# Performance work log

Hardware: AMD Instinct MI355X
Metric: run time of the kernel (lower is better)

## Reference

```python
import jax, jax.numpy as jnp
import numpy as np

NUM_HEADS = 8
EPS = 1e-12  # torch F.normalize default eps


def _l2_normalize(t, axis):
    n = jnp.sqrt(jnp.sum(t * t, axis=axis, keepdims=True))
    return t / jnp.maximum(n, EPS)


def setup_inputs() -> dict:
    key = jax.random.key(0)
    k1, k2, k3 = jax.random.split(key, 3)
    B, N, D = 32, 3136, 384
    x = jax.random.normal(k1, (B, N, D), dtype=jnp.float32)
    qkv_w = jax.random.normal(k2, (3 * D, D), dtype=jnp.float32) * (1.0 / np.sqrt(D))
    temperature = jnp.ones((NUM_HEADS, 1, 1), dtype=jnp.float32)
    proj_w = jax.random.normal(k3, (D, D), dtype=jnp.float32) * (1.0 / np.sqrt(D))
    proj_b = jnp.zeros((D,), dtype=jnp.float32)
    return {"x": x, "qkv_w": qkv_w, "temperature": temperature,
            "proj_w": proj_w, "proj_b": proj_b}


def reference(x, qkv_w, temperature, proj_w, proj_b):
    B, N, D = x.shape
    H = NUM_HEADS
    C = D // H
    # qkv projection (no bias), split last dim as (3, H, C) -> (3, B, H, C, N)
    qkv = jnp.einsum('bnd,ed->bne', x, qkv_w)
    qkv = qkv.reshape(B, N, 3, H, C).transpose(2, 0, 3, 4, 1)
    q, k, v = qkv[0], qkv[1], qkv[2]            # each (B, H, C, N)
    q = _l2_normalize(q, axis=-1)               # normalize over tokens N
    k = _l2_normalize(k, axis=-1)
    # cross-covariance attention: (B, H, C, C), scaled by per-head temperature
    attn = jnp.einsum('bhcn,bhdn->bhcd', q, k) * temperature
    attn = jax.nn.softmax(attn, axis=-1)
    out = jnp.einsum('bhcd,bhdn->bhcn', attn, v)  # (B, H, C, N)
    out = out.transpose(0, 3, 1, 2).reshape(B, N, D)
    return jnp.einsum('bnd,ed->bne', out, proj_w) + proj_b
```

## Files before the change

### kernel.cpp

```cpp
#include <hip/hip_runtime.h>


typedef __bf16 bf16x8 __attribute__((ext_vector_type(8)));
typedef float floatx4 __attribute__((ext_vector_type(4)));
typedef unsigned short u16;

#define B_ 32
#define N_ 3136
#define D_ 384
#define H_ 8
#define C_ 48
#define BN_ 100352

__device__ __forceinline__ u16 f2b(float f) {
  unsigned u = __builtin_bit_cast(unsigned, f);
  u += 0x7FFFu + ((u >> 16) & 1u);
  return (u16)(u >> 16);
}
__device__ __forceinline__ void gload16(const u16* g, u16* l) {
  __builtin_amdgcn_global_load_lds(
      (const __attribute__((address_space(1))) void*)g,
      (__attribute__((address_space(3))) void*)l, 16, 0, 0);
}

__global__ __launch_bounds__(256) void k_entry(const float* __restrict__ x,
                                               const float* __restrict__ qkv_w,
                                               const float* __restrict__ proj_w,
                                               u16* __restrict__ xbf,
                                               u16* __restrict__ xT,
                                               u16* __restrict__ wbf,
                                               u16* __restrict__ pwbf,
                                               u16* __restrict__ wvT) {
  int lin = blockIdx.x, t = threadIdx.x;
  if (lin < 9408) {
    int b = lin / 294, rem = lin % 294;
    int d0 = (rem / 49) * 64, n0 = (rem % 49) * 64;
    const float* xp = x + ((size_t)b * N_ + n0) * D_ + d0;
    __shared__ u16 L[64][68];
    int nl = t >> 4, dl = (t & 15) * 4;
#pragma unroll
    for (int p = 0; p < 4; p++) {
      int n = nl + p * 16;
      float4 v = *(const float4*)(xp + (size_t)n * D_ + dl);
      ushort4 o;
      o.x = f2b(v.x); o.y = f2b(v.y); o.z = f2b(v.z); o.w = f2b(v.w);
      *(ushort4*)(xbf + ((size_t)(b * N_ + n0 + n)) * D_ + d0 + dl) = o;
      *(ushort4*)(&L[n][dl]) = o;
    }
    __syncthreads();
    int dl2 = t >> 4, nl2 = (t & 15) * 4;
#pragma unroll
    for (int p = 0; p < 4; p++) {
      int d = dl2 + p * 16;
      ushort4 o;
      o.x = L[nl2 + 0][d]; o.y = L[nl2 + 1][d];
      o.z = L[nl2 + 2][d]; o.w = L[nl2 + 3][d];
      *(ushort4*)(xT + (size_t)(d0 + d) * BN_ + b * N_ + n0 + nl2) = o;
    }
  } else {
    int blk = lin - 9408;
    if (blk < 432) {
      int i = blk * 256 + t;
      float4 v = ((const float4*)qkv_w)[i];
      ushort4 o;
      o.x = f2b(v.x); o.y = f2b(v.y); o.z = f2b(v.z); o.w = f2b(v.w);
      ((ushort4*)wbf)[i] = o;
    } else if (blk < 576) {
      int i = (blk - 432) * 256 + t;
      float4 v = ((const float4*)proj_w)[i];
      ushort4 o;
      o.x = f2b(v.x); o.y = f2b(v.y); o.z = f2b(v.z); o.w = f2b(v.w);
      ((ushort4*)pwbf)[i] = o;
    } else {
      int h = blk - 576;
      for (int idx = t; idx < 384 * 64; idx += 256) {
        int j = idx >> 6, d = idx & 63;
        float v = (d < 48) ? qkv_w[(size_t)(2 * D_ + h * C_ + d) * D_ + j] : 0.f;
        wvT[(size_t)h * 24576 + idx] = f2b(v);
      }
    }
  }
}

__constant__ int c_ti[6] = {0, 0, 0, 1, 1, 2};
__constant__ int c_tj[6] = {0, 1, 2, 1, 2, 2};

__global__ __launch_bounds__(256) void k_gram(const u16* __restrict__ xT,
                                              float* __restrict__ G) {
  int lin = blockIdx.x;
  int w = (lin & 7) * 96 + (lin >> 3);
  int b = w / 24, rem = w % 24;
  int split = rem / 6, t6 = rem % 6;
  int m0 = c_ti[t6] * 128, n0 = c_tj[t6] * 128;
  int kbeg = split * 768, klen = (split == 3) ? 832 : 768;
  __shared__ u16 As[2][128][32];
  __shared__ u16 Bs[2][128][32];
  int t = threadIdx.x, wid = t >> 6, lane = t & 63;
  int srow = wid * 32 + (lane >> 2), scol = (lane & 3) * 8;
  int wm = (wid & 1) * 64, wn = (wid >> 1) * 64;
  int r = lane & 15, quad = lane >> 4, q8 = quad * 8;
  const u16* base = xT + (size_t)b * N_ + kbeg + scol;
  const u16* gA = base + (size_t)(m0 + srow) * BN_;
  const u16* gB = base + (size_t)(n0 + srow) * BN_;

  floatx4 acc[4][4] = {};
  for (int k0 = 0; k0 < klen; k0 += 64) {
#pragma unroll
    for (int ks = 0; ks < 2; ks++) {
      gload16(gA + k0 + ks * 32,                     &As[ks][wid * 32][0]);
      gload16(gA + k0 + ks * 32 + (size_t)16 * BN_,  &As[ks][wid * 32 + 16][0]);
      gload16(gB + k0 + ks * 32,                     &Bs[ks][wid * 32][0]);
      gload16(gB + k0 + ks * 32 + (size_t)16 * BN_,  &Bs[ks][wid * 32 + 16][0]);
    }
    __syncthreads();
#pragma unroll
    for (int ks = 0; ks < 2; ks++) {
      bf16x8 af[4], bf[4];
#pragma unroll
      for (int i = 0; i < 4; i++) af[i] = *(const bf16x8*)(&As[ks][wm + i * 16 + r][q8]);
#pragma unroll
      for (int j = 0; j < 4; j++) bf[j] = *(const bf16x8*)(&Bs[ks][wn + j * 16 + r][q8]);
#pragma unroll
      for (int i = 0; i < 4; i++)
#pragma unroll
        for (int j = 0; j < 4; j++)
          acc[i][j] = __builtin_amdgcn_mfma_f32_16x16x32_bf16(af[i], bf[j], acc[i][j], 0, 0, 0);
    }
    __syncthreads();
  }
  float* Gp = G + ((size_t)split * 192 + b * 6 + t6) * 16384;
#pragma unroll
  for (int i = 0; i < 4; i++)
#pragma unroll
    for (int j = 0; j < 4; j++)
#pragma unroll
      for (int v = 0; v < 4; v++) {
        int rr = wm + i * 16 + quad * 4 + v;
        int cc = wn + j * 16 + r;
        Gp[(size_t)rr * 128 + cc] = acc[i][j][v];
      }
}

__global__ __launch_bounds__(256) void k_gsum(const float* __restrict__ G,
                                              u16* __restrict__ Gbf) {
  int gid = blockIdx.x, t = threadIdx.x;
  int tb = gid >> 2, part = gid & 3;
  int b = tb / 6, t6 = tb % 6;
  int ti = c_ti[t6], tj = c_tj[t6];
  const float* G0 = G + ((size_t)b * 6 + t6) * 16384;
  u16* Gb = Gbf + (size_t)b * 147456;
#pragma unroll
  for (int it = 0; it < 4; it++) {
    int idx = part * 1024 + it * 256 + t;
    int i = idx >> 5, j4 = (idx & 31) * 4;
    float4 a = ((const float4*)G0)[idx];
    float4 c = ((const float4*)(G0 + (size_t)192 * 16384))[idx];
    float4 d = ((const float4*)(G0 + (size_t)384 * 16384))[idx];
    float4 e = ((const float4*)(G0 + (size_t)576 * 16384))[idx];
    float s0 = (a.x + c.x) + (d.x + e.x);
    float s1 = (a.y + c.y) + (d.y + e.y);
    float s2 = (a.z + c.z) + (d.z + e.z);
    float s3 = (a.w + c.w) + (d.w + e.w);
    ushort4 o;
    o.x = f2b(s0); o.y = f2b(s1); o.z = f2b(s2); o.w = f2b(s3);
    *(ushort4*)(Gb + (size_t)(ti * 128 + i) * 384 + tj * 128 + j4) = o;
    if (ti != tj) {
      int cbase = ti * 128 + i;
      Gb[(size_t)(tj * 128 + j4 + 0) * 384 + cbase] = o.x;
      Gb[(size_t)(tj * 128 + j4 + 1) * 384 + cbase] = o.y;
      Gb[(size_t)(tj * 128 + j4 + 2) * 384 + cbase] = o.z;
      Gb[(size_t)(tj * 128 + j4 + 3) * 384 + cbase] = o.w;
    }
  }
}

__global__ __launch_bounds__(256) void k_mid1(const u16* __restrict__ wbf,
                                              const u16* __restrict__ Gb,
                                              u16* __restrict__ Ubf) {
  int lin = blockIdx.x;
  int w = (lin & 7) * 72 + (lin >> 3);
  int b = w / 18, rem = w % 18;
  int m0 = (rem / 3) * 128, n0 = (rem % 3) * 128;
  __shared__ u16 As[2][128][32];
  __shared__ u16 Bs[2][128][32];
  int t = threadIdx.x, wid = t >> 6, lane = t & 63;
  int srow = wid * 32 + (lane >> 2), scol = (lane & 3) * 8;
  int wm = (wid & 1) * 64, wn = (wid >> 1) * 64;
  int r = lane & 15, quad = lane >> 4, q8 = quad * 8;
  const u16* gA = wbf + (size_t)(m0 + srow) * 384 + scol;
  const u16* gB = Gb + (size_t)b * 147456 + (size_t)(n0 + srow) * 384 + scol;

  floatx4 acc[4][4] = {};
  for (int k0 = 0; k0 < 384; k0 += 64) {
#pragma unroll
    for (int ks = 0; ks < 2; ks++) {
      gload16(gA + k0 + ks * 32,            &As[ks][wid * 32][0]);
      gload16(gA + k0 + ks * 32 + 16 * 384, &As[ks][wid * 32 + 16][0]);
      gload16(gB + k0 + ks * 32,            &Bs[ks][wid * 32][0]);
      gload16(gB + k0 + ks * 32 + 16 * 384, &Bs[ks][wid * 32 + 16][0]);
    }
    __syncthreads();
#pragma unroll
    for (int ks = 0; ks < 2; ks++) {
      bf16x8 af[4], bf[4];
#pragma unroll
      for (int i = 0; i < 4; i++) af[i] = *(const bf16x8*)(&As[ks][wm + i * 16 + r][q8]);
#pragma unroll
      for (int j = 0; j < 4; j++) bf[j] = *(const bf16x8*)(&Bs[ks][wn + j * 16 + r][q8]);
#pragma unroll
      for (int i = 0; i < 4; i++)
#pragma unroll
        for (int j = 0; j < 4; j++)
          acc[i][j] = __builtin_amdgcn_mfma_f32_16x16x32_bf16(af[i], bf[j], acc[i][j], 0, 0, 0);
    }
    __syncthreads();
  }
  u16* Ub = Ubf + (size_t)b * 294912;
#pragma unroll
  for (int i = 0; i < 4; i++)
#pragma unroll
    for (int j = 0; j < 4; j++)
#pragma unroll
      for (int v = 0; v < 4; v++) {
        int rr = m0 + wm + i * 16 + quad * 4 + v;
        int cc = n0 + wn + j * 16 + r;
        Ub[(size_t)rr * 384 + cc] = f2b(acc[i][j][v]);
      }
}

__global__ __launch_bounds__(256) void k_mid2(const u16* __restrict__ Ubf,
                                              const u16* __restrict__ wbf,
                                              const u16* __restrict__ wvT,
                                              const float* __restrict__ temp,
                                              u16* __restrict__ MT) {
  int bh = blockIdx.x, b = bh >> 3, h = bh & 7;
  __shared__ __align__(16) u16 sUq[48][32], sUk[48][32], sWq[48][32], sWk[48][32];
  __shared__ __align__(16) u16 sA[48][72];
  __shared__ float sSsq[96];
  __shared__ float sInv[96];
  int t = threadIdx.x, wid = t >> 6, lane = t & 63;
  int r = lane & 15, quad = lane >> 4, q8 = quad * 8;
  const u16* Uq = Ubf + (size_t)b * 294912 + (size_t)(h * C_) * 384;
  const u16* Uk = Ubf + (size_t)b * 294912 + (size_t)(D_ + h * C_) * 384;
  const u16* Wq = wbf + (size_t)(h * C_) * 384;
  const u16* Wk = wbf + (size_t)(D_ + h * C_) * 384;

  floatx4 accS[3] = {};
  floatx4 accD[6] = {};
  for (int k0 = 0; k0 < 384; k0 += 32) {
    for (int idx = t; idx < 768; idx += 256) {
      int tile = idx / 192, rem = idx - tile * 192;
      int rr = rem >> 2, c8 = (rem & 3) * 8;
      const u16* src = (tile == 0 ? Uq : tile == 1 ? Uk : tile == 2 ? Wq : Wk)
                       + (size_t)rr * 384 + k0 + c8;
      u16* dst = (tile == 0 ? &sUq[rr][c8] : tile == 1 ? &sUk[rr][c8]
                  : tile == 2 ? &sWq[rr][c8] : &sWk[rr][c8]);
      *(int4*)dst = *(const int4*)src;
    }
    __syncthreads();
    if (wid < 3) {
      bf16x8 uq = *(const bf16x8*)(&sUq[wid * 16 + r][q8]);
#pragma unroll
      for (int j = 0; j < 3; j++) {
        bf16x8 wk = *(const bf16x8*)(&sWk[j * 16 + r][q8]);
        accS[j] = __builtin_amdgcn_mfma_f32_16x16x32_bf16(uq, wk, accS[j], 0, 0, 0);
      }
    } else {
#pragma unroll
      for (int i = 0; i < 3; i++) {
        bf16x8 uq = *(const bf16x8*)(&sUq[i * 16 + r][q8]);
        bf16x8 wq = *(const bf16x8*)(&sWq[i * 16 + r][q8]);
        bf16x8 uk = *(const bf16x8*)(&sUk[i * 16 + r][q8]);
        bf16x8 wk = *(const bf16x8*)(&sWk[i * 16 + r][q8]);
        accD[i]     = __builtin_amdgcn_mfma_f32_16x16x32_bf16(uq, wq, accD[i], 0, 0, 0);
        accD[3 + i] = __builtin_amdgcn_mfma_f32_16x16x32_bf16(uk, wk, accD[3 + i], 0, 0, 0);
      }
    }
    __syncthreads();
  }
  if (wid == 3) {
#pragma unroll
    for (int i = 0; i < 3; i++)
#pragma unroll
      for (int v = 0; v < 4; v++)
        if (r == quad * 4 + v) {
          sSsq[i * 16 + r] = accD[i][v];
          sSsq[48 + i * 16 + r] = accD[3 + i][v];
        }
  }
  __syncthreads();
  if (t < 96) sInv[t] = 1.f / fmaxf(sqrtf(sSsq[t]), 1e-12f);
  __syncthreads();
  for (int idx = t; idx < 48 * 16; idx += 256) sA[idx >> 4][48 + (idx & 15)] = 0;
  float T = temp[h];
  if (wid < 3) {
    float L[3][4];
    int c_base = wid * 16 + quad * 4;
#pragma unroll
    for (int j = 0; j < 3; j++)
#pragma unroll
      for (int v = 0; v < 4; v++)
        L[j][v] = accS[j][v] * sInv[c_base + v] * sInv[48 + j * 16 + r] * T;
    float mx[4], sum[4];
#pragma unroll
    for (int v = 0; v < 4; v++) mx[v] = fmaxf(fmaxf(L[0][v], L[1][v]), L[2][v]);
#pragma unroll
    for (int m = 1; m <= 8; m <<= 1)
#pragma unroll
      for (int v = 0; v < 4; v++) mx[v] = fmaxf(mx[v], __shfl_xor(mx[v], m));
#pragma unroll
    for (int v = 0; v < 4; v++) sum[v] = 0.f;
#pragma unroll
    for (int j = 0; j < 3; j++)
#pragma unroll
      for (int v = 0; v < 4; v++) { L[j][v] = __expf(L[j][v] - mx[v]); sum[v] += L[j][v]; }
#pragma unroll
    for (int m = 1; m <= 8; m <<= 1)
#pragma unroll
      for (int v = 0; v < 4; v++) sum[v] += __shfl_xor(sum[v], m);
#pragma unroll
    for (int j = 0; j < 3; j++)
#pragma unroll
      for (int v = 0; v < 4; v++)
        sA[c_base + v][j * 16 + r] = f2b(L[j][v] / sum[v]);
  }
  __syncthreads();
  const u16* WvTh = wvT + (size_t)h * 24576;
  floatx4 accM[3][6] = {};
#pragma unroll
  for (int ks = 0; ks < 2; ks++) {
    bf16x8 af[3];
#pragma unroll
    for (int i = 0; i < 3; i++) af[i] = *(const bf16x8*)(&sA[i * 16 + r][ks * 32 + q8]);
#pragma unroll
    for (int jj = 0; jj < 6; jj++) {
      int j = wid * 96 + jj * 16 + r;
      bf16x8 bb = *(const bf16x8*)(WvTh + (size_t)j * 64 + ks * 32 + q8);
#pragma unroll
      for (int i = 0; i < 3; i++)
        accM[i][jj] = __builtin_amdgcn_mfma_f32_16x16x32_bf16(af[i], bb, accM[i][jj], 0, 0, 0);
    }
  }
  u16* MTb = MT + (size_t)b * 147456;
#pragma unroll
  for (int i = 0; i < 3; i++)
#pragma unroll
    for (int jj = 0; jj < 6; jj++)
#pragma unroll
      for (int v = 0; v < 4; v++) {
        int c = i * 16 + quad * 4 + v;
        int j = wid * 96 + jj * 16 + r;
        MTb[(size_t)j * 384 + h * C_ + c] = f2b(accM[i][jj][v]);
      }
}

__global__ __launch_bounds__(256) void k_mid3(const u16* __restrict__ pwbf,
                                              const u16* __restrict__ MT,
                                              u16* __restrict__ R) {
  int m0 = (blockIdx.x % 3) * 128, n0 = (blockIdx.x / 3) * 128, b = blockIdx.y;
  __shared__ u16 As[2][128][32];
  __shared__ u16 Bs[2][128][32];
  int t = threadIdx.x, wid = t >> 6, lane = t & 63;
  int srow = wid * 32 + (lane >> 2), scol = (lane & 3) * 8;
  int wm = (wid & 1) * 64, wn = (wid >> 1) * 64;
  int r = lane & 15, quad = lane >> 4, q8 = quad * 8;
  const u16* gA = pwbf + (size_t)(m0 + srow) * 384 + scol;
  const u16* gB = MT + (size_t)b * 147456 + (size_t)(n0 + srow) * 384 + scol;

  floatx4 acc[4][4] = {};
  for (int k0 = 0; k0 < 384; k0 += 64) {
#pragma unroll
    for (int ks = 0; ks < 2; ks++) {
      gload16(gA + k0 + ks * 32,            &As[ks][wid * 32][0]);
      gload16(gA + k0 + ks * 32 + 16 * 384, &As[ks][wid * 32 + 16][0]);
      gload16(gB + k0 + ks * 32,            &Bs[ks][wid * 32][0]);
      gload16(gB + k0 + ks * 32 + 16 * 384, &Bs[ks][wid * 32 + 16][0]);
    }
    __syncthreads();
#pragma unroll
    for (int ks = 0; ks < 2; ks++) {
      bf16x8 af[4], bf[4];
#pragma unroll
      for (int i = 0; i < 4; i++) af[i] = *(const bf16x8*)(&As[ks][wm + i * 16 + r][q8]);
#pragma unroll
      for (int j = 0; j < 4; j++) bf[j] = *(const bf16x8*)(&Bs[ks][wn + j * 16 + r][q8]);
#pragma unroll
      for (int i = 0; i < 4; i++)
#pragma unroll
        for (int j = 0; j < 4; j++)
          acc[i][j] = __builtin_amdgcn_mfma_f32_16x16x32_bf16(af[i], bf[j], acc[i][j], 0, 0, 0);
    }
    __syncthreads();
  }
  u16* Rb = R + (size_t)b * 147456;
#pragma unroll
  for (int i = 0; i < 4; i++)
#pragma unroll
    for (int j = 0; j < 4; j++)
#pragma unroll
      for (int v = 0; v < 4; v++) {
        int rr = m0 + wm + i * 16 + quad * 4 + v;
        int cc = n0 + wn + j * 16 + r;
        Rb[(size_t)rr * 384 + cc] = f2b(acc[i][j][v]);
      }
}

__global__ __launch_bounds__(256) void k_final(const u16* __restrict__ xbf,
                                               const u16* __restrict__ R,
                                               const float* __restrict__ bias,
                                               float* __restrict__ Y) {
  int lin = blockIdx.x;
  int w = (lin & 7) * 300 + (lin >> 3);
  int ft = w % 3, rest = w / 3;
  int b = rest / 25, gt = rest % 25;
  size_t g0 = (size_t)b * N_ + gt * 128;
  int f0 = ft * 128;
  __shared__ u16 As[2][128][32];
  __shared__ u16 Bs[2][128][32];
  int t = threadIdx.x, wid = t >> 6, lane = t & 63;
  int srow = wid * 32 + (lane >> 2), scol = (lane & 3) * 8;
  int wm = (wid & 1) * 64, wn = (wid >> 1) * 64;
  int r = lane & 15, quad = lane >> 4, q8 = quad * 8;
  const u16* gA = xbf + (g0 + srow) * 384 + scol;
  const u16* gB = R + (size_t)b * 147456 + (size_t)(f0 + srow) * 384 + scol;

  floatx4 acc[4][4] = {};
  for (int k0 = 0; k0 < 384; k0 += 64) {
#pragma unroll
    for (int ks = 0; ks < 2; ks++) {
      gload16(gA + k0 + ks * 32,            &As[ks][wid * 32][0]);
      gload16(gA + k0 + ks * 32 + 16 * 384, &As[ks][wid * 32 + 16][0]);
      gload16(gB + k0 + ks * 32,            &Bs[ks][wid * 32][0]);
      gload16(gB + k0 + ks * 32 + 16 * 384, &Bs[ks][wid * 32 + 16][0]);
    }
    __syncthreads();
#pragma unroll
    for (int ks = 0; ks < 2; ks++) {
      bf16x8 af[4], bf[4];
#pragma unroll
      for (int i = 0; i < 4; i++) af[i] = *(const bf16x8*)(&As[ks][wm + i * 16 + r][q8]);
#pragma unroll
      for (int j = 0; j < 4; j++) bf[j] = *(const bf16x8*)(&Bs[ks][wn + j * 16 + r][q8]);
#pragma unroll
      for (int i = 0; i < 4; i++)
#pragma unroll
        for (int j = 0; j < 4; j++)
          acc[i][j] = __builtin_amdgcn_mfma_f32_16x16x32_bf16(af[i], bf[j], acc[i][j], 0, 0, 0);
    }
    __syncthreads();
  }
#pragma unroll
  for (int i = 0; i < 4; i++)
#pragma unroll
    for (int j = 0; j < 4; j++) {
      int cc = f0 + wn + j * 16 + r;
      float bv = bias[cc];
#pragma unroll
      for (int v = 0; v < 4; v++) {
        int rr = wm + i * 16 + quad * 4 + v;
        if (gt * 128 + rr < N_)
          Y[(g0 + rr) * 384 + cc] = acc[i][j][v] + bv;
      }
    }
}

extern "C" void kernel_launch(void* const* d_in, const int* in_sizes, int n_in,
                              void* d_out, int out_size, void* d_ws, size_t ws_size,
                              hipStream_t stream) {
  const float* x      = (const float*)d_in[0];
  const float* qkv_w  = (const float*)d_in[1];
  const float* temp   = (const float*)d_in[2];
  const float* proj_w = (const float*)d_in[3];
  const float* proj_b = (const float*)d_in[4];
  float* out = (float*)d_out;

  char* ws = (char*)d_ws;
  u16*   xbf  = (u16*)(ws);
  u16*   xT   = (u16*)(ws + 77070336);
  u16*   wbf  = (u16*)(ws + 154140672);
  u16*   pwbf = (u16*)(ws + 155025408);
  u16*   wvT  = (u16*)(ws + 155320320);
  float* G    = (float*)(ws + 155713536);
  u16*   Gbf  = (u16*)(ws + 206045184);
  u16*   Ubf  = (u16*)(ws + 215482368);
  u16*   MT   = (u16*)(ws + 234356736);
  u16*   R    = (u16*)(ws + 243793920);

  k_entry<<<9992, 256, 0, stream>>>(x, qkv_w, proj_w, xbf, xT, wbf, pwbf, wvT);
  k_gram<<<768, 256, 0, stream>>>(xT, G);
  k_gsum<<<768, 256, 0, stream>>>(G, Gbf);
  k_mid1<<<576, 256, 0, stream>>>(wbf, Gbf, Ubf);
  k_mid2<<<256, 256, 0, stream>>>(Ubf, wbf, wvT, temp, MT);
  k_mid3<<<dim3(9, 32), 256, 0, stream>>>(pwbf, MT, R);
  k_final<<<2400, 256, 0, stream>>>(xbf, R, proj_b, out);
}
```

Measured before the change: 486.1 us.

## Split x conversion and transpose into kernels; stage final output through LDS

The fused conversion+transpose entry kernel becomes two kernels. One does a flat vectorized fp32-to-bf16 conversion of x. The other transposes the bf16 copy using 256-token tiles and 16-byte stores. The final GEMM epilogue now stages accumulators plus bias in LDS, then writes coalesced float4 rows instead of scattered scalar stores. This is meant to cut uncoalesced global writes. The cost is an extra launch, rereading the bf16 x (~77MB), and extra barriers in the epilogue.

```diff
diff --git a/kernel.cpp b/kernel.cpp
--- a/kernel.cpp
+++ b/kernel.cpp
@@ -23,42 +23,26 @@
       (__attribute__((address_space(3))) void*)l, 16, 0, 0);
 }
 
-__global__ __launch_bounds__(256) void k_entry(const float* __restrict__ x,
-                                               const float* __restrict__ qkv_w,
-                                               const float* __restrict__ proj_w,
-                                               u16* __restrict__ xbf,
-                                               u16* __restrict__ xT,
-                                               u16* __restrict__ wbf,
-                                               u16* __restrict__ pwbf,
-                                               u16* __restrict__ wvT) {
+__global__ __launch_bounds__(256) void k_cvt(const float* __restrict__ x,
+                                             const float* __restrict__ qkv_w,
+                                             const float* __restrict__ proj_w,
+                                             u16* __restrict__ xbf,
+                                             u16* __restrict__ wbf,
+                                             u16* __restrict__ pwbf,
+                                             u16* __restrict__ wvT) {
   int lin = blockIdx.x, t = threadIdx.x;
-  if (lin < 9408) {
-    int b = lin / 294, rem = lin % 294;
-    int d0 = (rem / 49) * 64, n0 = (rem % 49) * 64;
-    const float* xp = x + ((size_t)b * N_ + n0) * D_ + d0;
-    __shared__ u16 L[64][68];
-    int nl = t >> 4, dl = (t & 15) * 4;
-#pragma unroll
-    for (int p = 0; p < 4; p++) {
-      int n = nl + p * 16;
-      float4 v = *(const float4*)(xp + (size_t)n * D_ + dl);
+  if (lin < 4704) {
+    int base = lin * 256 + t;
+#pragma unroll
+    for (int k = 0; k < 8; k++) {
+      int i = base + k * 1204224;
+      float4 v = ((const float4*)x)[i];
       ushort4 o;
       o.x = f2b(v.x); o.y = f2b(v.y); o.z = f2b(v.z); o.w = f2b(v.w);
-      *(ushort4*)(xbf + ((size_t)(b * N_ + n0 + n)) * D_ + d0 + dl) = o;
-      *(ushort4*)(&L[n][dl]) = o;
-    }
-    __syncthreads();
-    int dl2 = t >> 4, nl2 = (t & 15) * 4;
-#pragma unroll
-    for (int p = 0; p < 4; p++) {
-      int d = dl2 + p * 16;
-      ushort4 o;
-      o.x = L[nl2 + 0][d]; o.y = L[nl2 + 1][d];
-      o.z = L[nl2 + 2][d]; o.w = L[nl2 + 3][d];
-      *(ushort4*)(xT + (size_t)(d0 + d) * BN_ + b * N_ + n0 + nl2) = o;
+      ((ushort4*)xbf)[i] = o;
     }
   } else {
-    int blk = lin - 9408;
+    int blk = lin - 4704;
     if (blk < 432) {
       int i = blk * 256 + t;
       float4 v = ((const float4*)qkv_w)[i];
@@ -78,6 +62,58 @@
         float v = (d < 48) ? qkv_w[(size_t)(2 * D_ + h * C_ + d) * D_ + j] : 0.f;
         wvT[(size_t)h * 24576 + idx] = f2b(v);
       }
+    }
+  }
+}
+
+__global__ __launch_bounds__(256) void k_tr(const u16* __restrict__ xbf,
+                                            u16* __restrict__ xT) {
+  __shared__ __align__(16) u16 L[64][264];
+  int lin = blockIdx.x, t = threadIdx.x;
+  int b = lin / 78, rem = lin % 78;
+  int dt = rem / 13, nt = rem % 13;
+  int d0 = dt * 64;
+  if (nt < 12) {
+    int n0 = nt * 256;
+    const u16* src0 = xbf + (size_t)(b * N_ + n0) * 384 + d0;
+#pragma unroll
+    for (int p = 0; p < 8; p++) {
+      int nrow = (t >> 3) + p * 32;
+      int dseg = (t & 7) * 8;
+      int4 v = *(const int4*)(src0 + (size_t)nrow * 384 + dseg);
+      const u16* pv = (const u16*)&v;
+#pragma unroll
+      for (int k = 0; k < 8; k++) L[dseg + k][nrow] = pv[k];
+    }
+    __syncthreads();
+    u16* dst0 = xT + (size_t)d0 * BN_ + b * N_ + n0;
+#pragma unroll
+    for (int p = 0; p < 8; p++) {
+      int d = (t >> 5) + p * 8;
+      int nseg = (t & 31) * 8;
+      int4 v = *(const int4*)(&L[d][nseg]);
+      *(int4*)(dst0 + (size_t)d * BN_ + nseg) = v;
+    }
+  } else {
+    int n0 = 3072;
+    const u16* src0 = xbf + (size_t)(b * N_ + n0) * 384 + d0;
+#pragma unroll
+    for (int p = 0; p < 2; p++) {
+      int nrow = (t >> 3) + p * 32;
+      int dseg = (t & 7) * 8;
+      int4 v = *(const int4*)(src0 + (size_t)nrow * 384 + dseg);
+      const u16* pv = (const u16*)&v;
+#pragma unroll
+      for (int k = 0; k < 8; k++) L[dseg + k][nrow] = pv[k];
+    }
+    __syncthreads();
+    u16* dst0 = xT + (size_t)d0 * BN_ + b * N_ + n0;
+#pragma unroll
+    for (int p = 0; p < 2; p++) {
+      int d = (t >> 3) + p * 32;
+      int nseg = (t & 7) * 8;
+      int4 v = *(const int4*)(&L[d][nseg]);
+      *(int4*)(dst0 + (size_t)d * BN_ + nseg) = v;
     }
   }
 }
@@ -415,8 +451,9 @@
   int b = rest / 25, gt = rest % 25;
   size_t g0 = (size_t)b * N_ + gt * 128;
   int f0 = ft * 128;
-  __shared__ u16 As[2][128][32];
-  __shared__ u16 Bs[2][128][32];
+  __shared__ __align__(16) u16 smem[16384];
+  u16 (*As)[128][32] = (u16(*)[128][32])smem;
+  u16 (*Bs)[128][32] = (u16(*)[128][32])(smem + 8192);
   int t = threadIdx.x, wid = t >> 6, lane = t & 63;
   int srow = wid * 32 + (lane >> 2), scol = (lane & 3) * 8;
   int wm = (wid & 1) * 64, wn = (wid >> 1) * 64;
@@ -449,19 +486,34 @@
     }
     __syncthreads();
   }
-#pragma unroll
-  for (int i = 0; i < 4; i++)
-#pragma unroll
-    for (int j = 0; j < 4; j++) {
-      int cc = f0 + wn + j * 16 + r;
-      float bv = bias[cc];
-#pragma unroll
-      for (int v = 0; v < 4; v++) {
-        int rr = wm + i * 16 + quad * 4 + v;
-        if (gt * 128 + rr < N_)
-          Y[(g0 + rr) * 384 + cc] = acc[i][j][v] + bv;
-      }
-    }
+  float* Lf = (float*)smem;
+#pragma unroll
+  for (int h = 0; h < 2; h++) {
+    __syncthreads();
+    if ((wid & 1) == h) {
+#pragma unroll
+      for (int i = 0; i < 4; i++)
+#pragma unroll
+        for (int j = 0; j < 4; j++) {
+          int cc = wn + j * 16 + r;
+          float bv = bias[f0 + cc];
+#pragma unroll
+          for (int v = 0; v < 4; v++)
+            Lf[(i * 16 + quad * 4 + v) * 128 + cc] = acc[i][j][v] + bv;
+        }
+    }
+    __syncthreads();
+#pragma unroll
+    for (int p = 0; p < 8; p++) {
+      int row = (t >> 5) + p * 8;
+      int grow = h * 64 + row;
+      int col = (t & 31) * 4;
+      if (gt * 128 + grow < N_) {
+        float4 vv = *(const float4*)(&Lf[row * 128 + col]);
+        *(float4*)(&Y[(g0 + grow) * 384 + f0 + col]) = vv;
+      }
+    }
+  }
 }
 
 extern "C" void kernel_launch(void* const* d_in, const int* in_sizes, int n_in,
@@ -486,7 +538,8 @@
   u16*   MT   = (u16*)(ws + 234356736);
   u16*   R    = (u16*)(ws + 243793920);
 
-  k_entry<<<9992, 256, 0, stream>>>(x, qkv_w, proj_w, xbf, xT, wbf, pwbf, wvT);
+  k_cvt<<<5288, 256, 0, stream>>>(x, qkv_w, proj_w, xbf, wbf, pwbf, wvT);
+  k_tr<<<2496, 256, 0, stream>>>(xbf, xT);
   k_gram<<<768, 256, 0, stream>>>(xT, G);
   k_gsum<<<768, 256, 0, stream>>>(G, Gbf);
   k_mid1<<<576, 256, 0, stream>>>(wbf, Gbf, Ubf);
```

After: 475.5 us. 2.2% less time.
